# Kernel optimization log

Hardware: AMD Instinct MI355X
Metric: run time of the kernel (lower is better)

Reference implementation:

```python
import jax, jax.numpy as jnp
import numpy as np

B, P, O, C = 64, 8732, 32, 81
IMG = 224.0
THRESH = 0.5
NEG_POS = 3.0
ALPHA = 1.0


def cxcy_to_xy(b):
    return jnp.concatenate([b[..., :2] - b[..., 2:] / 2, b[..., :2] + b[..., 2:] / 2], -1)


def xy_to_cxcy(b):
    return jnp.concatenate([(b[..., :2] + b[..., 2:]) / 2, b[..., 2:] - b[..., :2]], -1)


def coco_to_xy(b):  # [x, y, w, h] -> [xmin, ymin, xmax, ymax]
    return jnp.concatenate([b[..., :2], b[..., :2] + b[..., 2:]], -1)


def cxcy_to_gcxgcy(cxcy, priors):  # SSD offset encoding, variances 10 / 5
    g_cxcy = (cxcy[..., :2] - priors[..., :2]) / (priors[..., 2:] / 10.0)
    g_wh = jnp.log(cxcy[..., 2:] / priors[..., 2:]) * 5.0
    return jnp.concatenate([g_cxcy, g_wh], -1)


def pairwise_iou(a, b):  # a: [O,4] xy, b: [P,4] xy -> [O,P]
    lt = jnp.maximum(a[:, None, :2], b[None, :, :2])
    rb = jnp.minimum(a[:, None, 2:], b[None, :, 2:])
    wh = jnp.clip(rb - lt, 0.0)
    inter = wh[..., 0] * wh[..., 1]
    area_a = (a[:, 2] - a[:, 0]) * (a[:, 3] - a[:, 1])
    area_b = (b[:, 2] - b[:, 0]) * (b[:, 3] - b[:, 1])
    return inter / (area_a[:, None] + area_b[None, :] - inter)


def setup_inputs() -> dict:
    key = jax.random.key(0)
    k1, k2, k3, k4, k5, k6, k7 = jax.random.split(key, 7)
    pred_locs = jax.random.normal(k1, (B, P, 4), dtype=jnp.float32)
    pred_scores = jax.random.normal(k2, (B, P, C), dtype=jnp.float32)
    # COCO-format gt boxes [x, y, w, h] in pixel coords, guaranteed inside image
    xy = jax.random.uniform(k3, (B, O, 2), minval=0.0, maxval=IMG * 0.55)
    wh = jax.random.uniform(k4, (B, O, 2), minval=8.0, maxval=IMG * 0.4)
    gt_boxes = jnp.concatenate([xy, wh], -1)
    gt_labels = jax.random.randint(k5, (B, O), 1, C)  # foreground labels 1..C-1
    p_cxcy = jax.random.uniform(k6, (P, 2), minval=0.05, maxval=0.95)
    p_wh = jax.random.uniform(k7, (P, 2), minval=0.05, maxval=0.5)
    priors_cxcy = jnp.concatenate([p_cxcy, p_wh], -1)
    return {"pred_locs": pred_locs, "pred_scores": pred_scores,
            "gt_boxes": gt_boxes, "gt_labels": gt_labels,
            "priors_cxcy": priors_cxcy}


def reference(pred_locs, pred_scores, gt_boxes, gt_labels, priors_cxcy):
    priors_xy = cxcy_to_xy(priors_cxcy)

    def match(boxes_coco, labels):  # one image: [O,4] coco, [O] int
        boxes_xy = coco_to_xy(boxes_coco) / IMG  # normalize to [0,1]
        ov = pairwise_iou(boxes_xy, priors_xy)  # [O, P]
        overlap_for_prior = ov.max(axis=0)       # [P]
        object_for_prior = ov.argmax(axis=0)     # [P]
        prior_for_object = ov.argmax(axis=1)     # [O]
        # force each object to claim its best prior
        object_for_prior = object_for_prior.at[prior_for_object].set(jnp.arange(O))
        overlap_for_prior = overlap_for_prior.at[prior_for_object].set(1.0)
        label_for_prior = labels[object_for_prior]
        label_for_prior = jnp.where(overlap_for_prior < THRESH, 0, label_for_prior)
        true_locs = cxcy_to_gcxgcy(xy_to_cxcy(boxes_xy[object_for_prior]), priors_cxcy)
        return true_locs, label_for_prior

    true_locs, true_classes = jax.vmap(match)(gt_boxes, gt_labels)  # [B,P,4], [B,P]

    positive = true_classes != 0          # [B, P]
    n_pos = positive.sum(axis=1)          # [B]
    n_pos_cl = jnp.maximum(n_pos, 1).astype(jnp.float32)
    n_hard_neg = NEG_POS * n_pos_cl

    # SmoothL1 (beta=1), mean over positive prior coords
    diff = jnp.abs(pred_locs - true_locs)
    sl1 = jnp.where(diff < 1.0, 0.5 * diff * diff, diff - 0.5)  # [B,P,4]
    total_pos = n_pos.sum()
    loc_loss = jnp.where(
        total_pos > 0,
        jnp.where(positive[..., None], sl1, 0.0).sum()
        / jnp.maximum(total_pos * 4, 1).astype(jnp.float32),
        0.0,
    )

    # per-prior cross entropy
    logp = jax.nn.log_softmax(pred_scores, axis=-1)
    ce = -jnp.take_along_axis(logp, true_classes[..., None], axis=-1)[..., 0]  # [B,P]

    conf_pos_sum = jnp.where(positive, ce, 0.0).sum()
    ce_neg = jnp.where(positive, 0.0, ce)
    ce_neg_sorted = -jnp.sort(-ce_neg, axis=1)  # descending per image
    ranks = jnp.arange(P)[None, :]
    hard = ranks < n_hard_neg[:, None]
    conf_hard_neg_sum = jnp.where(hard, ce_neg_sorted, 0.0).sum()

    conf_loss = (conf_hard_neg_sum + conf_pos_sum) / n_pos_cl.sum()
    return conf_loss + ALPHA * loc_loss
```

## Files before the change

kernel.cpp:

```cpp
#include <hip/hip_runtime.h>
#include <cstdint>
#include <cstddef>

#define BB 64
#define PP 8732
#define OO 32
#define CC 81
#define NBM 35
#define NBG 35
#define TR 64

__global__ __launch_bounds__(256) void k_match(
    const float* __restrict__ gt_boxes,
    const float4* __restrict__ priors,
    float* __restrict__ ovl, int* __restrict__ obj,
    unsigned long long* __restrict__ part)
{
    int b = blockIdx.y, blk = blockIdx.x;
    int tid = threadIdx.x;
    int p = blk * 256 + tid;
    bool pv = p < PP;
    __shared__ float bx1[OO], by1[OO], bx2[OO], by2[OO], bar[OO];
    __shared__ float mat[OO][264];
    __shared__ unsigned long long po[OO][8];
    if (tid < OO) {
        const float* g = gt_boxes + ((size_t)b * OO + tid) * 4;
        float x1 = g[0] / 224.0f, y1 = g[1] / 224.0f;
        float x2 = (g[0] + g[2]) / 224.0f, y2 = (g[1] + g[3]) / 224.0f;
        bx1[tid] = x1; by1[tid] = y1; bx2[tid] = x2; by2[tid] = y2;
        bar[tid] = (x2 - x1) * (y2 - y1);
    }
    __syncthreads();
    float4 pr = priors[pv ? p : 0];
    float px1 = pr.x - pr.z * 0.5f, py1 = pr.y - pr.w * 0.5f;
    float px2 = pr.x + pr.z * 0.5f, py2 = pr.y + pr.w * 0.5f;
    float parea = (px2 - px1) * (py2 - py1);
    float best = -1.0f; int bo = 0;
    #pragma unroll
    for (int o = 0; o < OO; ++o) {
        float lx = fmaxf(bx1[o], px1), ly = fmaxf(by1[o], py1);
        float rx = fminf(bx2[o], px2), ry = fminf(by2[o], py2);
        float w = fmaxf(rx - lx, 0.0f), h = fmaxf(ry - ly, 0.0f);
        float inter = w * h;
        float iou = inter / (bar[o] + parea - inter);
        iou = pv ? iou : 0.0f;
        mat[o][tid] = iou;
        if (iou > best) { best = iou; bo = o; }
    }
    if (pv) {
        size_t idx = (size_t)b * PP + p;
        ovl[idx] = best;
        obj[idx] = bo;
    }
    __syncthreads();
    {
        int o = tid >> 3, j = tid & 7;
        float bv = -1.0f; int bt = 0;
        #pragma unroll
        for (int k = 0; k < 32; ++k) {
            int t = j + 8 * k;
            float v = mat[o][t];
            if (v > bv) { bv = v; bt = t; }
        }
        unsigned pg = (unsigned)(blk * 256 + bt);
        po[o][j] = ((unsigned long long)__float_as_uint(bv) << 32)
                 | (unsigned long long)(0xFFFFFFFFu - pg);
    }
    __syncthreads();
    if (tid < OO) {
        unsigned long long m = po[tid][0];
        #pragma unroll
        for (int j = 1; j < 8; ++j) if (po[tid][j] > m) m = po[tid][j];
        part[((size_t)b * NBM + blk) * OO + tid] = m;
    }
}

__global__ void k_force(const unsigned long long* __restrict__ part,
                        float* __restrict__ ovl, int* __restrict__ obj)
{
    int b = blockIdx.x;
    __shared__ int s_pfo[OO];
    int t = threadIdx.x;
    if (t < OO) {
        unsigned long long m = part[((size_t)b * NBM + 0) * OO + t];
        for (int blk = 1; blk < NBM; ++blk) {
            unsigned long long v = part[((size_t)b * NBM + blk) * OO + t];
            if (v > m) m = v;
        }
        s_pfo[t] = (int)(0xFFFFFFFFu - (unsigned)(m & 0xFFFFFFFFull));
    }
    __syncthreads();
    if (t == 0) {
        for (int o = 0; o < OO; ++o) {
            int p = s_pfo[o];
            obj[(size_t)b * PP + p] = o;
            ovl[(size_t)b * PP + p] = 1.0f;
        }
    }
}

__global__ __launch_bounds__(256) void k_lse(
    const float* __restrict__ scores,
    float* __restrict__ lse, float* __restrict__ xbg)
{
    int b = blockIdx.y;
    int p0 = blockIdx.x * TR;
    int nrows = PP - p0; if (nrows > TR) nrows = TR;
    int n4 = nrows * CC / 4;
    __shared__ float4 sv4[TR * CC / 4];
    const float4* src = (const float4*)(scores + ((size_t)b * PP + p0) * CC);
    for (int i = threadIdx.x; i < n4; i += 256) sv4[i] = src[i];
    __syncthreads();
    const float* sv = (const float*)sv4;
    int g = threadIdx.x >> 4, l = threadIdx.x & 15;
    #pragma unroll
    for (int rr = 0; rr < 4; ++rr) {
        int r = g * 4 + rr;
        if (r >= nrows) break;
        const float* row = sv + r * CC;
        float se = 0.f;
        #pragma unroll
        for (int k = 0; k < 6; ++k) {
            int c = l + 16 * k;
            if (c < CC) se += __expf(row[c]);
        }
        #pragma unroll
        for (int s = 8; s >= 1; s >>= 1) se += __shfl_xor(se, s, 16);
        if (l == 0) {
            size_t idx = (size_t)b * PP + p0 + r;
            lse[idx] = __logf(se);
            xbg[idx] = row[0];
        }
    }
}

__global__ __launch_bounds__(256) void k_gather(
    const float* __restrict__ scores,
    const float4* __restrict__ pred_locs,
    const float* __restrict__ gt_boxes,
    const int* __restrict__ gt_labels,
    const float4* __restrict__ priors,
    const float* __restrict__ ovl, const int* __restrict__ obj,
    const float* __restrict__ lse, const float* __restrict__ xbg,
    float* __restrict__ ceneg,
    float* __restrict__ pp_posce, float* __restrict__ pp_sl1,
    int* __restrict__ pp_np)
{
    int b = blockIdx.y;
    int p = blockIdx.x * 256 + threadIdx.x;
    __shared__ float s_posce, s_sl1;
    __shared__ int s_np;
    if (threadIdx.x == 0) { s_posce = 0.f; s_sl1 = 0.f; s_np = 0; }
    __syncthreads();
    if (p < PP) {
        size_t idx = (size_t)b * PP + p;
        float ov = ovl[idx];
        int ob = obj[idx];
        int lab = (ov < 0.5f) ? 0 : gt_labels[b * OO + ob];
        float L = lse[idx];
        float cn;
        if (lab == 0) {
            cn = fmaxf(L - xbg[idx], 0.0f);
        } else {
            float x = scores[idx * CC + lab];
            float ce = fmaxf(L - x, 0.0f);
            cn = 0.f;
            float4 pl = pred_locs[idx];
            float4 pq = priors[p];
            const float* g = gt_boxes + ((size_t)b * OO + ob) * 4;
            float x1 = g[0] / 224.0f, y1 = g[1] / 224.0f;
            float x2 = (g[0] + g[2]) / 224.0f, y2 = (g[1] + g[3]) / 224.0f;
            float cx = (x1 + x2) * 0.5f, cy = (y1 + y2) * 0.5f;
            float w = x2 - x1, h = y2 - y1;
            float tx = (cx - pq.x) / (pq.z / 10.0f);
            float ty = (cy - pq.y) / (pq.w / 10.0f);
            float tw = __logf(w / pq.z) * 5.0f;
            float th = __logf(h / pq.w) * 5.0f;
            float d0 = fabsf(pl.x - tx), d1 = fabsf(pl.y - ty);
            float d2 = fabsf(pl.z - tw), d3 = fabsf(pl.w - th);
            float sl = (d0 < 1.f ? 0.5f * d0 * d0 : d0 - 0.5f)
                     + (d1 < 1.f ? 0.5f * d1 * d1 : d1 - 0.5f)
                     + (d2 < 1.f ? 0.5f * d2 * d2 : d2 - 0.5f)
                     + (d3 < 1.f ? 0.5f * d3 * d3 : d3 - 0.5f);
            atomicAdd(&s_posce, ce);
            atomicAdd(&s_sl1, sl);
            atomicAdd(&s_np, 1);
        }
        ceneg[idx] = cn;
    }
    __syncthreads();
    if (threadIdx.x == 0) {
        int slot = b * NBG + blockIdx.x;
        pp_posce[slot] = s_posce;
        pp_sl1[slot]   = s_sl1;
        pp_np[slot]    = s_np;
    }
}

__global__ __launch_bounds__(512) void k_topk(
    const float* __restrict__ ceneg,
    const float* __restrict__ pp_posce, const float* __restrict__ pp_sl1,
    const int* __restrict__ pp_np,
    float* __restrict__ hard, float* __restrict__ posce_b,
    float* __restrict__ sl1_b, int* __restrict__ n_pos)
{
    int b = blockIdx.x, tid = threadIdx.x;
    __shared__ float4 sv4[PP / 4];
    __shared__ int s_i[8];
    __shared__ float s_f[8], s_f2[8];
    __shared__ int s_bcast;
    float pc = 0.f, sl = 0.f; int np = 0;
    for (int i = tid; i < NBG; i += 512) {
        pc += pp_posce[b * NBG + i];
        sl += pp_sl1[b * NBG + i];
        np += pp_np[b * NBG + i];
    }
    #pragma unroll
    for (int s = 32; s >= 1; s >>= 1) {
        pc += __shfl_xor(pc, s, 64);
        sl += __shfl_xor(sl, s, 64);
        np += __shfl_xor(np, s, 64);
    }
    int wid = tid >> 6;
    if ((tid & 63) == 0) { s_i[wid] = np; s_f[wid] = pc; s_f2[wid] = sl; }
    const float4* src = (const float4*)(ceneg + (size_t)b * PP);
    for (int i = tid; i < PP / 4; i += 512) sv4[i] = src[i];
    __syncthreads();
    if (tid == 0) {
        int n = 0; float fp = 0.f, fs = 0.f;
        #pragma unroll
        for (int k = 0; k < 8; ++k) { n += s_i[k]; fp += s_f[k]; fs += s_f2[k]; }
        n_pos[b] = n; posce_b[b] = fp; sl1_b[b] = fs;
        s_bcast = n;
    }
    __syncthreads();
    np = s_bcast;
    int K = 3 * (np > 1 ? np : 1);
    if (K > PP) K = PP;
    unsigned lo = 0u, hi = 0x7F800000u;
    while (hi - lo > 1u) {
        unsigned mid = (lo + hi) >> 1;
        float t = __uint_as_float(mid);
        int c = 0;
        for (int i = tid; i < PP / 4; i += 512) {
            float4 q = sv4[i];
            c += (q.x >= t) + (q.y >= t) + (q.z >= t) + (q.w >= t);
        }
        #pragma unroll
        for (int s = 32; s >= 1; s >>= 1) c += __shfl_xor(c, s, 64);
        if ((tid & 63) == 0) s_i[wid] = c;
        __syncthreads();
        if (tid == 0) {
            int n = 0;
            #pragma unroll
            for (int k = 0; k < 8; ++k) n += s_i[k];
            s_bcast = n;
        }
        __syncthreads();
        int cnt = s_bcast;
        if (cnt >= K) lo = mid; else hi = mid;
        __syncthreads();
    }
    float vk = __uint_as_float(lo);
    float sm = 0.f; int cg = 0;
    for (int i = tid; i < PP / 4; i += 512) {
        float4 q = sv4[i];
        if (q.x > vk) { sm += q.x; cg++; }
        if (q.y > vk) { sm += q.y; cg++; }
        if (q.z > vk) { sm += q.z; cg++; }
        if (q.w > vk) { sm += q.w; cg++; }
    }
    #pragma unroll
    for (int s = 32; s >= 1; s >>= 1) {
        sm += __shfl_xor(sm, s, 64);
        cg += __shfl_xor(cg, s, 64);
    }
    if ((tid & 63) == 0) { s_f[wid] = sm; s_i[wid] = cg; }
    __syncthreads();
    if (tid == 0) {
        float S = 0.f; int CG = 0;
        #pragma unroll
        for (int k = 0; k < 8; ++k) { S += s_f[k]; CG += s_i[k]; }
        hard[b] = S + (float)(K - CG) * vk;
    }
}

__global__ void k_final(const int* __restrict__ n_pos, const float* __restrict__ hard,
                        const float* __restrict__ posce_b, const float* __restrict__ sl1_b,
                        float* __restrict__ out)
{
    int t = threadIdx.x;
    int np = (t < BB) ? n_pos[t] : 0;
    float h  = (t < BB) ? hard[t] : 0.f;
    float pc = (t < BB) ? posce_b[t] : 0.f;
    float sl = (t < BB) ? sl1_b[t] : 0.f;
    float cl = (t < BB) ? (float)(np > 1 ? np : 1) : 0.f;
    int tp = np; float hs = h; float cls = cl;
    #pragma unroll
    for (int s = 32; s >= 1; s >>= 1) {
        tp  += __shfl_xor(tp, s, 64);
        hs  += __shfl_xor(hs, s, 64);
        cls += __shfl_xor(cls, s, 64);
        pc  += __shfl_xor(pc, s, 64);
        sl  += __shfl_xor(sl, s, 64);
    }
    if (t == 0) {
        float conf = (hs + pc) / cls;
        float loc = 0.f;
        if (tp > 0) {
            int den = tp * 4; if (den < 1) den = 1;
            loc = sl / (float)den;
        }
        out[0] = conf + loc;
    }
}

extern "C" void kernel_launch(void* const* d_in, const int* in_sizes, int n_in,
                              void* d_out, int out_size, void* d_ws, size_t ws_size,
                              hipStream_t stream)
{
    const float* pred_locs   = (const float*)d_in[0];
    const float* pred_scores = (const float*)d_in[1];
    const float* gt_boxes    = (const float*)d_in[2];
    const int*   gt_labels   = (const int*)d_in[3];
    const float* priors      = (const float*)d_in[4];

    char* ws = (char*)d_ws;
    const size_t npf = (size_t)BB * PP;
    size_t off = 0;
    float* ovl   = (float*)(ws + off); off += 4 * npf;
    int*   obj   = (int*)  (ws + off); off += 4 * npf;
    float* ceneg = (float*)(ws + off); off += 4 * npf;
    float* lse   = (float*)(ws + off); off += 4 * npf;
    float* xbg   = (float*)(ws + off); off += 4 * npf;
    unsigned long long* part = (unsigned long long*)(ws + off); off += 8 * (size_t)BB * NBM * OO;
    float* pp_posce = (float*)(ws + off); off += 4 * (size_t)BB * NBG;
    float* pp_sl1   = (float*)(ws + off); off += 4 * (size_t)BB * NBG;
    int*   pp_np    = (int*)  (ws + off); off += 4 * (size_t)BB * NBG;
    float* posce_b  = (float*)(ws + off); off += 4 * BB;
    float* sl1_b    = (float*)(ws + off); off += 4 * BB;
    int*   n_pos    = (int*)  (ws + off); off += 4 * BB;
    float* hard     = (float*)(ws + off); off += 4 * BB;

    dim3 gL((PP + TR - 1) / TR, BB);
    k_lse<<<gL, 256, 0, stream>>>(pred_scores, lse, xbg);

    dim3 gM(NBM, BB);
    k_match<<<gM, 256, 0, stream>>>(gt_boxes, (const float4*)priors, ovl, obj, part);

    k_force<<<BB, 64, 0, stream>>>(part, ovl, obj);

    dim3 gG(NBG, BB);
    k_gather<<<gG, 256, 0, stream>>>(pred_scores, (const float4*)pred_locs, gt_boxes,
                                     gt_labels, (const float4*)priors, ovl, obj,
                                     lse, xbg, ceneg, pp_posce, pp_sl1, pp_np);

    k_topk<<<BB, 512, 0, stream>>>(ceneg, pp_posce, pp_sl1, pp_np,
                                   hard, posce_b, sl1_b, n_pos);

    k_final<<<1, 64, 0, stream>>>(n_pos, hard, posce_b, sl1_b, (float*)d_out);
}
```

Measured before the change: 326.7 us.

## Fuse log-sum-exp and CE gather into one kernel after matching

The separate log-sum-exp kernel and the gather kernel are merged into one k_ce kernel that runs after matching. Each block stages 64 score rows in shared memory, computes the row's log-sum-exp and picks out the target-class logit in the same pass, then writes ceneg and the per-block positive sums. This removes the lse/xbg intermediate arrays, one launch, and the second scattered read of scores for positive priors. In exchange, the large score read can no longer start before matching finishes, and the per-block partial arrays grow to 137 blocks per image.

```diff
diff --git a/kernel.cpp b/kernel.cpp
--- a/kernel.cpp
+++ b/kernel.cpp
@@ -7,8 +7,8 @@
 #define OO 32
 #define CC 81
 #define NBM 35
-#define NBG 35
 #define TR 64
+#define NBC 137
 
 __global__ __launch_bounds__(256) void k_match(
     const float* __restrict__ gt_boxes,
@@ -99,98 +99,95 @@
     }
 }
 
-__global__ __launch_bounds__(256) void k_lse(
-    const float* __restrict__ scores,
-    float* __restrict__ lse, float* __restrict__ xbg)
-{
-    int b = blockIdx.y;
-    int p0 = blockIdx.x * TR;
-    int nrows = PP - p0; if (nrows > TR) nrows = TR;
-    int n4 = nrows * CC / 4;
-    __shared__ float4 sv4[TR * CC / 4];
-    const float4* src = (const float4*)(scores + ((size_t)b * PP + p0) * CC);
-    for (int i = threadIdx.x; i < n4; i += 256) sv4[i] = src[i];
-    __syncthreads();
-    const float* sv = (const float*)sv4;
-    int g = threadIdx.x >> 4, l = threadIdx.x & 15;
-    #pragma unroll
-    for (int rr = 0; rr < 4; ++rr) {
-        int r = g * 4 + rr;
-        if (r >= nrows) break;
-        const float* row = sv + r * CC;
-        float se = 0.f;
-        #pragma unroll
-        for (int k = 0; k < 6; ++k) {
-            int c = l + 16 * k;
-            if (c < CC) se += __expf(row[c]);
-        }
-        #pragma unroll
-        for (int s = 8; s >= 1; s >>= 1) se += __shfl_xor(se, s, 16);
-        if (l == 0) {
-            size_t idx = (size_t)b * PP + p0 + r;
-            lse[idx] = __logf(se);
-            xbg[idx] = row[0];
-        }
-    }
-}
-
-__global__ __launch_bounds__(256) void k_gather(
+__global__ __launch_bounds__(256) void k_ce(
     const float* __restrict__ scores,
     const float4* __restrict__ pred_locs,
     const float* __restrict__ gt_boxes,
     const int* __restrict__ gt_labels,
     const float4* __restrict__ priors,
     const float* __restrict__ ovl, const int* __restrict__ obj,
-    const float* __restrict__ lse, const float* __restrict__ xbg,
     float* __restrict__ ceneg,
     float* __restrict__ pp_posce, float* __restrict__ pp_sl1,
     int* __restrict__ pp_np)
 {
     int b = blockIdx.y;
-    int p = blockIdx.x * 256 + threadIdx.x;
+    int p0 = blockIdx.x * TR;
+    int nrows = PP - p0; if (nrows > TR) nrows = TR;
+    int n4 = nrows * CC / 4;
+    __shared__ float4 sv4[TR * CC / 4];
+    __shared__ int s_lab[TR], s_ob[TR];
     __shared__ float s_posce, s_sl1;
     __shared__ int s_np;
-    if (threadIdx.x == 0) { s_posce = 0.f; s_sl1 = 0.f; s_np = 0; }
-    __syncthreads();
-    if (p < PP) {
-        size_t idx = (size_t)b * PP + p;
+    int tid = threadIdx.x;
+    if (tid == 0) { s_posce = 0.f; s_sl1 = 0.f; s_np = 0; }
+    if (tid < nrows) {
+        size_t idx = (size_t)b * PP + p0 + tid;
         float ov = ovl[idx];
         int ob = obj[idx];
-        int lab = (ov < 0.5f) ? 0 : gt_labels[b * OO + ob];
-        float L = lse[idx];
-        float cn;
-        if (lab == 0) {
-            cn = fmaxf(L - xbg[idx], 0.0f);
-        } else {
-            float x = scores[idx * CC + lab];
-            float ce = fmaxf(L - x, 0.0f);
-            cn = 0.f;
-            float4 pl = pred_locs[idx];
-            float4 pq = priors[p];
-            const float* g = gt_boxes + ((size_t)b * OO + ob) * 4;
-            float x1 = g[0] / 224.0f, y1 = g[1] / 224.0f;
-            float x2 = (g[0] + g[2]) / 224.0f, y2 = (g[1] + g[3]) / 224.0f;
-            float cx = (x1 + x2) * 0.5f, cy = (y1 + y2) * 0.5f;
-            float w = x2 - x1, h = y2 - y1;
-            float tx = (cx - pq.x) / (pq.z / 10.0f);
-            float ty = (cy - pq.y) / (pq.w / 10.0f);
-            float tw = __logf(w / pq.z) * 5.0f;
-            float th = __logf(h / pq.w) * 5.0f;
-            float d0 = fabsf(pl.x - tx), d1 = fabsf(pl.y - ty);
-            float d2 = fabsf(pl.z - tw), d3 = fabsf(pl.w - th);
-            float sl = (d0 < 1.f ? 0.5f * d0 * d0 : d0 - 0.5f)
-                     + (d1 < 1.f ? 0.5f * d1 * d1 : d1 - 0.5f)
-                     + (d2 < 1.f ? 0.5f * d2 * d2 : d2 - 0.5f)
-                     + (d3 < 1.f ? 0.5f * d3 * d3 : d3 - 0.5f);
-            atomicAdd(&s_posce, ce);
-            atomicAdd(&s_sl1, sl);
-            atomicAdd(&s_np, 1);
-        }
-        ceneg[idx] = cn;
-    }
-    __syncthreads();
-    if (threadIdx.x == 0) {
-        int slot = b * NBG + blockIdx.x;
+        s_ob[tid] = ob;
+        s_lab[tid] = (ov < 0.5f) ? 0 : gt_labels[b * OO + ob];
+    }
+    const float4* src = (const float4*)(scores + ((size_t)b * PP + p0) * CC);
+    for (int i = tid; i < n4; i += 256) sv4[i] = src[i];
+    __syncthreads();
+    const float* sv = (const float*)sv4;
+    int g = tid >> 4, l = tid & 15;
+    #pragma unroll
+    for (int rr = 0; rr < 4; ++rr) {
+        int r = g * 4 + rr;
+        if (r >= nrows) break;
+        int lab = s_lab[r];
+        const float* row = sv + r * CC;
+        float se = 0.f, xl = 0.f;
+        #pragma unroll
+        for (int k = 0; k < 6; ++k) {
+            int c = l + 16 * k;
+            if (c < CC) {
+                float x = row[c];
+                se += __expf(x);
+                if (c == lab) xl = x;
+            }
+        }
+        #pragma unroll
+        for (int s = 8; s >= 1; s >>= 1) {
+            se += __shfl_xor(se, s, 16);
+            xl += __shfl_xor(xl, s, 16);
+        }
+        if (l == 0) {
+            int p = p0 + r;
+            size_t idx = (size_t)b * PP + p;
+            float ce = fmaxf(__logf(se) - xl, 0.0f);
+            float cn = ce;
+            if (lab != 0) {
+                cn = 0.f;
+                int ob = s_ob[r];
+                float4 pl = pred_locs[idx];
+                float4 pq = priors[p];
+                const float* gg = gt_boxes + ((size_t)b * OO + ob) * 4;
+                float x1 = gg[0] / 224.0f, y1 = gg[1] / 224.0f;
+                float x2 = (gg[0] + gg[2]) / 224.0f, y2 = (gg[1] + gg[3]) / 224.0f;
+                float cx = (x1 + x2) * 0.5f, cy = (y1 + y2) * 0.5f;
+                float w = x2 - x1, h = y2 - y1;
+                float tx = (cx - pq.x) / (pq.z / 10.0f);
+                float ty = (cy - pq.y) / (pq.w / 10.0f);
+                float tw = __logf(w / pq.z) * 5.0f;
+                float th = __logf(h / pq.w) * 5.0f;
+                float d0 = fabsf(pl.x - tx), d1 = fabsf(pl.y - ty);
+                float d2 = fabsf(pl.z - tw), d3 = fabsf(pl.w - th);
+                float sl = (d0 < 1.f ? 0.5f * d0 * d0 : d0 - 0.5f)
+                         + (d1 < 1.f ? 0.5f * d1 * d1 : d1 - 0.5f)
+                         + (d2 < 1.f ? 0.5f * d2 * d2 : d2 - 0.5f)
+                         + (d3 < 1.f ? 0.5f * d3 * d3 : d3 - 0.5f);
+                atomicAdd(&s_posce, ce);
+                atomicAdd(&s_sl1, sl);
+                atomicAdd(&s_np, 1);
+            }
+            ceneg[idx] = cn;
+        }
+    }
+    __syncthreads();
+    if (tid == 0) {
+        int slot = b * NBC + blockIdx.x;
         pp_posce[slot] = s_posce;
         pp_sl1[slot]   = s_sl1;
         pp_np[slot]    = s_np;
@@ -210,10 +207,10 @@
     __shared__ float s_f[8], s_f2[8];
     __shared__ int s_bcast;
     float pc = 0.f, sl = 0.f; int np = 0;
-    for (int i = tid; i < NBG; i += 512) {
-        pc += pp_posce[b * NBG + i];
-        sl += pp_sl1[b * NBG + i];
-        np += pp_np[b * NBG + i];
+    for (int i = tid; i < NBC; i += 512) {
+        pc += pp_posce[b * NBC + i];
+        sl += pp_sl1[b * NBC + i];
+        np += pp_np[b * NBC + i];
     }
     #pragma unroll
     for (int s = 32; s >= 1; s >>= 1) {
@@ -331,29 +328,24 @@
     float* ovl   = (float*)(ws + off); off += 4 * npf;
     int*   obj   = (int*)  (ws + off); off += 4 * npf;
     float* ceneg = (float*)(ws + off); off += 4 * npf;
-    float* lse   = (float*)(ws + off); off += 4 * npf;
-    float* xbg   = (float*)(ws + off); off += 4 * npf;
     unsigned long long* part = (unsigned long long*)(ws + off); off += 8 * (size_t)BB * NBM * OO;
-    float* pp_posce = (float*)(ws + off); off += 4 * (size_t)BB * NBG;
-    float* pp_sl1   = (float*)(ws + off); off += 4 * (size_t)BB * NBG;
-    int*   pp_np    = (int*)  (ws + off); off += 4 * (size_t)BB * NBG;
+    float* pp_posce = (float*)(ws + off); off += 4 * (size_t)BB * NBC;
+    float* pp_sl1   = (float*)(ws + off); off += 4 * (size_t)BB * NBC;
+    int*   pp_np    = (int*)  (ws + off); off += 4 * (size_t)BB * NBC;
     float* posce_b  = (float*)(ws + off); off += 4 * BB;
     float* sl1_b    = (float*)(ws + off); off += 4 * BB;
     int*   n_pos    = (int*)  (ws + off); off += 4 * BB;
     float* hard     = (float*)(ws + off); off += 4 * BB;
 
-    dim3 gL((PP + TR - 1) / TR, BB);
-    k_lse<<<gL, 256, 0, stream>>>(pred_scores, lse, xbg);
-
     dim3 gM(NBM, BB);
     k_match<<<gM, 256, 0, stream>>>(gt_boxes, (const float4*)priors, ovl, obj, part);
 
     k_force<<<BB, 64, 0, stream>>>(part, ovl, obj);
 
-    dim3 gG(NBG, BB);
-    k_gather<<<gG, 256, 0, stream>>>(pred_scores, (const float4*)pred_locs, gt_boxes,
-                                     gt_labels, (const float4*)priors, ovl, obj,
-                                     lse, xbg, ceneg, pp_posce, pp_sl1, pp_np);
+    dim3 gC(NBC, BB);
+    k_ce<<<gC, 256, 0, stream>>>(pred_scores, (const float4*)pred_locs, gt_boxes,
+                                 gt_labels, (const float4*)priors, ovl, obj,
+                                 ceneg, pp_posce, pp_sl1, pp_np);
 
     k_topk<<<BB, 512, 0, stream>>>(ceneg, pp_posce, pp_sl1, pp_np,
                                    hard, posce_b, sl1_b, n_pos);
```

New measurement: 327.0 us. Within noise of the previous version (+0.1%).
